# Optimization experiments

Hardware: AMD Instinct MI355X
Metric: run time of the kernel (lower is better)

Reference implementation:

```python
import jax, jax.numpy as jnp
import numpy as np

B, N, D = 16, 1024, 768
H = 12
HD = D // H
HID = 4 * D
EPS = 1e-6


def _layernorm(x, g, b):
    mu = jnp.mean(x, axis=-1, keepdims=True)
    var = jnp.mean(jnp.square(x - mu), axis=-1, keepdims=True)
    return (x - mu) * jax.lax.rsqrt(var + EPS) * g + b


def setup_inputs() -> dict:
    key = jax.random.key(0)
    ks = jax.random.split(key, 8)
    s_d = 1.0 / np.sqrt(D)
    s_h = 1.0 / np.sqrt(HID)
    return {
        "x": jax.random.normal(ks[0], (B, N, D), dtype=jnp.float32),
        "qkv_w": jax.random.uniform(ks[1], (3 * D, D), jnp.float32, -s_d, s_d),
        "proj_w": jax.random.uniform(ks[2], (D, D), jnp.float32, -s_d, s_d),
        "proj_b": jax.random.uniform(ks[3], (D,), jnp.float32, -s_d, s_d),
        "fc1_w": jax.random.uniform(ks[4], (HID, D), jnp.float32, -s_d, s_d),
        "fc1_b": jax.random.uniform(ks[5], (HID,), jnp.float32, -s_d, s_d),
        "fc2_w": jax.random.uniform(ks[6], (D, HID), jnp.float32, -s_h, s_h),
        "fc2_b": jax.random.uniform(ks[7], (D,), jnp.float32, -s_h, s_h),
        "norm1_g": jnp.ones((D,), jnp.float32),
        "norm1_b": jnp.zeros((D,), jnp.float32),
        "norm2_g": jnp.ones((D,), jnp.float32),
        "norm2_b": jnp.zeros((D,), jnp.float32),
    }


def _attention(x, qkv_w, proj_w, proj_b):
    b, n, _ = x.shape
    qkv = x @ qkv_w.T                                  # [b,n,3D] (no bias: qkv_bias=False)
    qkv = qkv.reshape(b, n, 3, H, HD)
    q, k, v = (jnp.transpose(qkv[:, :, i], (0, 2, 1, 3)) for i in range(3))  # [b,h,n,hd]
    scale = HD ** (-0.5)
    dots = jnp.einsum("bhid,bhjd->bhij", q, k) * scale
    attn = jax.nn.softmax(dots, axis=-1)
    out = jnp.einsum("bhij,bhjd->bhid", attn, v)
    out = jnp.transpose(out, (0, 2, 1, 3)).reshape(b, n, H * HD)
    return out @ proj_w.T + proj_b


def _mlp(x, fc1_w, fc1_b, fc2_w, fc2_b):
    h = jax.nn.gelu(x @ fc1_w.T + fc1_b, approximate=False)
    return h @ fc2_w.T + fc2_b


def reference(x, qkv_w, proj_w, proj_b, fc1_w, fc1_b, fc2_w, fc2_b,
              norm1_g, norm1_b, norm2_g, norm2_b):
    x = x + _attention(_layernorm(x, norm1_g, norm1_b), qkv_w, proj_w, proj_b)
    x = x + _mlp(_layernorm(x, norm2_g, norm2_b), fc1_w, fc1_b, fc2_w, fc2_b)
    return x
```

## Files before the change

kernel.cpp:

```cpp
#include <hip/hip_runtime.h>
#include <hip/hip_bf16.h>
#include <math.h>

using bf16 = __hip_bfloat16;
typedef __attribute__((ext_vector_type(8))) short short8;
typedef __attribute__((ext_vector_type(4))) short shortx4;
typedef __attribute__((ext_vector_type(4))) float floatx4;

#define BB 16
#define NN 1024
#define DD 768
#define HH 12
#define HD 64
#define HID 3072

__device__ __forceinline__ floatx4 mfma_bf16(short8 a, short8 b, floatx4 c) {
  return __builtin_amdgcn_mfma_f32_16x16x32_bf16(a, b, c, 0, 0, 0);
}

__device__ __forceinline__ short bf16_bits(float f) {
  union { bf16 h; short s; } u;
  u.h = __float2bfloat16(f);
  return u.s;
}

__device__ __forceinline__ void async_copy16(const void* g, void* l) {
  __builtin_amdgcn_global_load_lds(
      (const __attribute__((address_space(1))) unsigned int*)g,
      (__attribute__((address_space(3))) unsigned int*)l,
      16, 0, 0);
}

__global__ __launch_bounds__(256)
void cvt_kernel(const float* __restrict__ in, bf16* __restrict__ out, int n4)
{
  const int i = blockIdx.x * 256 + threadIdx.x;
  if (i >= n4) return;
  const float4 v = ((const float4*)in)[i];
  shortx4 o;
  o.x = bf16_bits(v.x); o.y = bf16_bits(v.y);
  o.z = bf16_bits(v.z); o.w = bf16_bits(v.w);
  ((shortx4*)out)[i] = o;
}

__global__ __launch_bounds__(256)
void ln_kernel(const float* __restrict__ x, const float* __restrict__ g,
               const float* __restrict__ b, bf16* __restrict__ y)
{
  const int row = blockIdx.x;
  const int t = threadIdx.x;
  const float* xr = x + (size_t)row * DD;
  float v[3];
  float s = 0.f, s2 = 0.f;
#pragma unroll
  for (int i = 0; i < 3; ++i) {
    float f = xr[t + i * 256];
    v[i] = f;
    s += f;
    s2 += f * f;
  }
#pragma unroll
  for (int off = 1; off < 64; off <<= 1) {
    s  += __shfl_xor(s, off);
    s2 += __shfl_xor(s2, off);
  }
  __shared__ float red[2][4];
  const int wave = t >> 6, lane = t & 63;
  if (lane == 0) { red[0][wave] = s; red[1][wave] = s2; }
  __syncthreads();
  s  = red[0][0] + red[0][1] + red[0][2] + red[0][3];
  s2 = red[1][0] + red[1][1] + red[1][2] + red[1][3];
  const float mu = s * (1.f / DD);
  const float var = s2 * (1.f / DD) - mu * mu;
  const float inv = rsqrtf(var + 1e-6f);
  bf16* yr = y + (size_t)row * DD;
#pragma unroll
  for (int i = 0; i < 3; ++i) {
    int c = t + i * 256;
    yr[c] = __float2bfloat16((v[i] - mu) * inv * g[c] + b[c]);
  }
}

template <int EPI>
__global__ __launch_bounds__(256, 4)
void gemm_kernel(const bf16* __restrict__ A, const bf16* __restrict__ W,
                 const float* __restrict__ bias, const float* __restrict__ res,
                 void* __restrict__ Cv, int N, int K)
{
  __shared__ __align__(16) short smem[16896];
  short* sA = smem;
  short* sB = smem + 8192;

  const int tid  = threadIdx.x;
  const int lane = tid & 63;
  const int wave = tid >> 6;
  const int wm = wave & 1, wn = wave >> 1;
  const int row16 = lane & 15, quad = lane >> 4;

  const int lin = blockIdx.y * gridDim.x + blockIdx.x;
  const int per = gridDim.x * 8;
  const int pan = lin / per, rem = lin % per;
  const int bm = (pan * 8 + (rem & 7)) * 128;
  const int bn = (rem >> 3) * 128;

  const int lrow = lane >> 3;
  const int lkc  = (lane & 7) ^ lrow;

  const bf16* Ag = A + (size_t)(bm + wave * 32 + lrow) * K + lkc * 8;
  const bf16* Bg = W + (size_t)(bn + wave * 32 + lrow) * K + lkc * 8;
  short* sAw = sA + wave * 2048;
  short* sBw = sB + wave * 2048;

  floatx4 acc[4][4] = {};

  for (int kt = 0; kt < K; kt += 64) {
#pragma unroll
    for (int g = 0; g < 4; ++g) {
      async_copy16(Ag + (size_t)g * 8 * K + kt, sAw + g * 512);
      async_copy16(Bg + (size_t)g * 8 * K + kt, sBw + g * 512);
    }
    __syncthreads();
#pragma unroll
    for (int c = 0; c < 2; ++c) {
      short8 af[4], bfr[4];
      const int kc = c * 4 + quad;
#pragma unroll
      for (int mt = 0; mt < 4; ++mt) {
        const int row = wm * 64 + mt * 16 + row16;
        af[mt] = *(const short8*)&sA[(row >> 3) * 512 + ((row & 7) * 8 + (kc ^ (row & 7))) * 8];
      }
#pragma unroll
      for (int nt = 0; nt < 4; ++nt) {
        const int row = wn * 64 + nt * 16 + row16;
        bfr[nt] = *(const short8*)&sB[(row >> 3) * 512 + ((row & 7) * 8 + (kc ^ (row & 7))) * 8];
      }
#pragma unroll
      for (int mt = 0; mt < 4; ++mt)
#pragma unroll
        for (int nt = 0; nt < 4; ++nt)
          acc[mt][nt] = mfma_bf16(bfr[nt], af[mt], acc[mt][nt]);
    }
    __syncthreads();
  }

  if (EPI == 1) {
#pragma unroll
    for (int mt = 0; mt < 4; ++mt) {
      const int row = bm + wm * 64 + mt * 16 + row16;
#pragma unroll
      for (int nt = 0; nt < 4; ++nt) {
        const int col = bn + wn * 64 + nt * 16 + quad * 4;
        const floatx4 bv = *(const floatx4*)&bias[col];
        const floatx4 rv = *(const floatx4*)&res[(size_t)row * N + col];
        floatx4 o;
#pragma unroll
        for (int r = 0; r < 4; ++r) o[r] = acc[mt][nt][r] + bv[r] + rv[r];
        *(floatx4*)&((float*)Cv)[(size_t)row * N + col] = o;
      }
    }
  } else {
    short* sC = smem;
#pragma unroll
    for (int mt = 0; mt < 4; ++mt) {
      const int lr = wm * 64 + mt * 16 + row16;
#pragma unroll
      for (int nt = 0; nt < 4; ++nt) {
        const int lc = wn * 64 + nt * 16 + quad * 4;
        floatx4 bv = {};
        if (EPI == 2) bv = *(const floatx4*)&bias[bn + lc];
        shortx4 pk;
#pragma unroll
        for (int r = 0; r < 4; ++r) {
          float v = acc[mt][nt][r] + bv[r];
          if (EPI == 2) v = 0.5f * v * (1.f + erff(v * 0.70710678118f));
          pk[r] = bf16_bits(v);
        }
        *(shortx4*)&sC[lr * 132 + lc] = pk;
      }
    }
    __syncthreads();
#pragma unroll
    for (int it = 0; it < 8; ++it) {
      const int row = (tid >> 4) + it * 16;
      const int col = (tid & 15) * 8;
      short8 v = *(const short8*)&sC[row * 132 + col];
      *(short8*)&((bf16*)Cv)[(size_t)(bm + row) * N + bn + col] = v;
    }
  }
}

__global__ __launch_bounds__(256)
void vtrans_kernel(const bf16* __restrict__ qkv, bf16* __restrict__ vt)
{
  const int bh = blockIdx.y;
  const int b = bh / HH, h = bh % HH;
  const int n0 = blockIdx.x * 64;
  __shared__ __align__(16) short tile[64 * 72];
  const int tid = threadIdx.x;

  const int r = tid >> 2, c16 = (tid & 3) * 16;
  const bf16* src = qkv + (size_t)(b * NN + n0 + r) * 2304 + 2 * DD + h * 64 + c16;
  *(short8*)&tile[r * 72 + c16]     = *(const short8*)(src);
  *(short8*)&tile[r * 72 + c16 + 8] = *(const short8*)(src + 8);
  __syncthreads();

#pragma unroll
  for (int it = 0; it < 2; ++it) {
    const int d  = (tid >> 3) + it * 32;
    const int jg = (tid & 7) * 8;
    short8 o;
#pragma unroll
    for (int t = 0; t < 8; ++t) ((short*)&o)[t] = tile[(jg + t) * 72 + d];
    *(short8*)&vt[((size_t)bh * 64 + d) * NN + n0 + jg] = o;
  }
}

__global__ __launch_bounds__(256, 2)
void attn_kernel(const bf16* __restrict__ qkv, const bf16* __restrict__ vt,
                 bf16* __restrict__ out)
{
  const int bh = blockIdx.y;
  const int b = bh / HH, h = bh % HH;
  const int q0 = blockIdx.x * 128;
  const int tid = threadIdx.x;
  const int lane = tid & 63;
  const int wave = tid >> 6;
  const int row16 = lane & 15, quad = lane >> 4;

  __shared__ __align__(16) short sK[64 * 72];
  __shared__ __align__(16) short sVt[64 * 72];
  __shared__ __align__(16) short sP[4][32 * 72];

  const bf16* base  = qkv + (size_t)b * NN * 2304 + h * 64;
  const bf16* vbase = vt + (size_t)bh * 64 * NN;

  short8 qf[2][2];
#pragma unroll
  for (int qg = 0; qg < 2; ++qg) {
    const bf16* qrow = base + (size_t)(q0 + wave * 32 + qg * 16 + row16) * 2304;
    qf[qg][0] = *(const short8*)(qrow + quad * 8);
    qf[qg][1] = *(const short8*)(qrow + 32 + quad * 8);
  }

  floatx4 o_acc[2][4] = {};
  floatx4 l_acc[2] = {};
  const short8 ones = { (short)0x3F80, (short)0x3F80, (short)0x3F80, (short)0x3F80,
                        (short)0x3F80, (short)0x3F80, (short)0x3F80, (short)0x3F80 };

  const int sr = tid >> 2;
  const int sc = (tid & 3) * 16;
  const float ESC = 0.1803368801f;

  for (int jt = 0; jt < NN / 64; ++jt) {
    const int j0 = jt * 64;
    {
      const bf16* kp = base + (size_t)(j0 + sr) * 2304 + DD + sc;
      *(short8*)&sK[sr * 72 + sc]     = *(const short8*)(kp);
      *(short8*)&sK[sr * 72 + sc + 8] = *(const short8*)(kp + 8);
      const bf16* vp = vbase + (size_t)sr * NN + j0 + sc;
      *(short8*)&sVt[sr * 72 + sc]     = *(const short8*)(vp);
      *(short8*)&sVt[sr * 72 + sc + 8] = *(const short8*)(vp + 8);
    }
    __syncthreads();

#pragma unroll
    for (int nt = 0; nt < 4; ++nt) {
      short8 kb0 = *(const short8*)&sK[(nt * 16 + row16) * 72 + quad * 8];
      short8 kb1 = *(const short8*)&sK[(nt * 16 + row16) * 72 + 32 + quad * 8];
#pragma unroll
      for (int qg = 0; qg < 2; ++qg) {
        floatx4 st = {};
        st = mfma_bf16(kb0, qf[qg][0], st);
        st = mfma_bf16(kb1, qf[qg][1], st);
        shortx4 pk;
#pragma unroll
        for (int r = 0; r < 4; ++r)
          pk[r] = bf16_bits(exp2f(fminf(st[r] * ESC, 30.f)));
        *(shortx4*)&sP[wave][(qg * 16 + row16) * 72 + nt * 16 + quad * 4] = pk;
      }
    }

    short8 vb[4][2];
#pragma unroll
    for (int dt = 0; dt < 4; ++dt) {
      vb[dt][0] = *(const short8*)&sVt[(dt * 16 + row16) * 72 + quad * 8];
      vb[dt][1] = *(const short8*)&sVt[(dt * 16 + row16) * 72 + 32 + quad * 8];
    }
#pragma unroll
    for (int qg = 0; qg < 2; ++qg) {
      short8 pf0 = *(const short8*)&sP[wave][(qg * 16 + row16) * 72 + quad * 8];
      short8 pf1 = *(const short8*)&sP[wave][(qg * 16 + row16) * 72 + 32 + quad * 8];
      l_acc[qg] = mfma_bf16(pf0, ones, l_acc[qg]);
      l_acc[qg] = mfma_bf16(pf1, ones, l_acc[qg]);
#pragma unroll
      for (int dt = 0; dt < 4; ++dt) {
        o_acc[qg][dt] = mfma_bf16(pf0, vb[dt][0], o_acc[qg][dt]);
        o_acc[qg][dt] = mfma_bf16(pf1, vb[dt][1], o_acc[qg][dt]);
      }
    }
    __syncthreads();
  }

#pragma unroll
  for (int qg = 0; qg < 2; ++qg) {
#pragma unroll
    for (int r = 0; r < 4; ++r) {
      const float inv = 1.f / l_acc[qg][r];
      const size_t n = (size_t)(b * NN + q0 + wave * 32 + qg * 16 + quad * 4 + r);
#pragma unroll
      for (int dt = 0; dt < 4; ++dt) {
        out[n * DD + h * 64 + dt * 16 + row16] =
            __float2bfloat16(o_acc[qg][dt][r] * inv);
      }
    }
  }
}

extern "C" void kernel_launch(void* const* d_in, const int* in_sizes, int n_in,
                              void* d_out, int out_size, void* d_ws, size_t ws_size,
                              hipStream_t stream)
{
  const float* x       = (const float*)d_in[0];
  const float* qkv_w   = (const float*)d_in[1];
  const float* proj_w  = (const float*)d_in[2];
  const float* proj_b  = (const float*)d_in[3];
  const float* fc1_w   = (const float*)d_in[4];
  const float* fc1_b   = (const float*)d_in[5];
  const float* fc2_w   = (const float*)d_in[6];
  const float* fc2_b   = (const float*)d_in[7];
  const float* norm1_g = (const float*)d_in[8];
  const float* norm1_b = (const float*)d_in[9];
  const float* norm2_g = (const float*)d_in[10];
  const float* norm2_b = (const float*)d_in[11];
  float* out = (float*)d_out;

  const int M = BB * NN;
  char* ws = (char*)d_ws;

  bf16* wq = (bf16*)ws;
  bf16* wp = wq + (size_t)3 * DD * DD;
  bf16* w1 = wp + (size_t)DD * DD;
  bf16* w2 = w1 + (size_t)HID * DD;
  bf16* xn = w2 + (size_t)DD * HID;
  char* p2 = (char*)(xn + (size_t)M * DD);
  const size_t base_b = (size_t)(p2 - ws);

  int NBc = 1;
  for (int c = 16; c >= 1; c >>= 1)
    if (ws_size >= base_b + (size_t)c * 1024 * 7680) { NBc = c; break; }

  const int Rc = NBc * NN;
  bf16* qkvb = (bf16*)p2;
  bf16* aob  = qkvb + (size_t)Rc * 2304;
  bf16* vtb  = aob  + (size_t)Rc * DD;
  bf16* hb   = (bf16*)p2;

  cvt_kernel<<<(3 * DD * DD / 4 + 255) / 256, 256, 0, stream>>>(qkv_w, wq, 3 * DD * DD / 4);
  cvt_kernel<<<(DD * DD / 4 + 255) / 256, 256, 0, stream>>>(proj_w, wp, DD * DD / 4);
  cvt_kernel<<<(HID * DD / 4 + 255) / 256, 256, 0, stream>>>(fc1_w, w1, HID * DD / 4);
  cvt_kernel<<<(DD * HID / 4 + 255) / 256, 256, 0, stream>>>(fc2_w, w2, DD * HID / 4);

  ln_kernel<<<M, 256, 0, stream>>>(x, norm1_g, norm1_b, xn);

  for (int c = 0; c < BB / NBc; ++c) {
    const size_t r0 = (size_t)c * Rc;
    gemm_kernel<0><<<dim3(3 * DD / 128, Rc / 128), 256, 0, stream>>>(
        xn + r0 * DD, wq, nullptr, nullptr, qkvb, 3 * DD, DD);
    vtrans_kernel<<<dim3(NN / 64, NBc * HH), 256, 0, stream>>>(qkvb, vtb);
    attn_kernel<<<dim3(NN / 128, NBc * HH), 256, 0, stream>>>(qkvb, vtb, aob);
    gemm_kernel<1><<<dim3(DD / 128, Rc / 128), 256, 0, stream>>>(
        aob, wp, proj_b, x + r0 * DD, out + r0 * DD, DD, DD);
  }

  ln_kernel<<<M, 256, 0, stream>>>(out, norm2_g, norm2_b, xn);

  for (int c = 0; c < BB / NBc; ++c) {
    const size_t r0 = (size_t)c * Rc;
    gemm_kernel<2><<<dim3(HID / 128, Rc / 128), 256, 0, stream>>>(
        xn + r0 * DD, w1, fc1_b, nullptr, hb, HID, DD);
    gemm_kernel<1><<<dim3(DD / 128, Rc / 128), 256, 0, stream>>>(
        hb, w2, fc2_b, out + r0 * DD, out + r0 * DD, DD, HID);
  }
}
```

Measured before the change: 556.0 us.

## Rewrite GEMM with 256x256 tiles, 4-stage async LDS pipeline, fast GELU

The GEMM kernel moves from 128x128 tiles with 256 threads and a single-buffered K loop to 256x256 tiles with 512 threads. It uses a 4-slot circular LDS buffer with async global-to-LDS copies, split barriers and s_setprio around the MFMA blocks, so loads for future K-steps overlap compute. The epilogue now writes directly to global memory instead of staging through LDS. The exact erf GELU is replaced by a sigmoid-style exp2/rcp approximation. The changes aim to hide load latency and cut epilogue and transcendental cost, at the price of 128KB LDS per block, fewer blocks in flight, and small numeric differences in GELU.

```diff
diff --git a/kernel.cpp b/kernel.cpp
--- a/kernel.cpp
+++ b/kernel.cpp
@@ -29,6 +29,12 @@
       (const __attribute__((address_space(1))) unsigned int*)g,
       (__attribute__((address_space(3))) unsigned int*)l,
       16, 0, 0);
+}
+
+__device__ __forceinline__ float gelu_f(float x) {
+  const float z = x * fmaf(0.10294324f, x * x, 2.3022082f);
+  const float e = exp2f(z);
+  return x - x * __builtin_amdgcn_rcpf(e + 1.0f);
 }
 
 __global__ __launch_bounds__(256)
@@ -82,109 +88,142 @@
 }
 
 template <int EPI>
-__global__ __launch_bounds__(256, 4)
+__global__ __launch_bounds__(512, 2)
 void gemm_kernel(const bf16* __restrict__ A, const bf16* __restrict__ W,
                  const float* __restrict__ bias, const float* __restrict__ res,
                  void* __restrict__ Cv, int N, int K)
 {
-  __shared__ __align__(16) short smem[16896];
-  short* sA = smem;
-  short* sB = smem + 8192;
+  __shared__ __align__(16) short smem[65536];
 
   const int tid  = threadIdx.x;
   const int lane = tid & 63;
-  const int wave = tid >> 6;
-  const int wm = wave & 1, wn = wave >> 1;
+  const int w    = tid >> 6;
+  const int wm   = w >> 2;
+  const int wn   = w & 3;
   const int row16 = lane & 15, quad = lane >> 4;
 
-  const int lin = blockIdx.y * gridDim.x + blockIdx.x;
-  const int per = gridDim.x * 8;
+  const int gx = gridDim.x, gy = gridDim.y;
+  const int lin = blockIdx.y * gx + blockIdx.x;
+  const int PP  = (gy & 7) ? gy : 8;
+  const int per = gx * PP;
   const int pan = lin / per, rem = lin % per;
-  const int bm = (pan * 8 + (rem & 7)) * 128;
-  const int bn = (rem >> 3) * 128;
-
-  const int lrow = lane >> 3;
-  const int lkc  = (lane & 7) ^ lrow;
-
-  const bf16* Ag = A + (size_t)(bm + wave * 32 + lrow) * K + lkc * 8;
-  const bf16* Bg = W + (size_t)(bn + wave * 32 + lrow) * K + lkc * 8;
-  short* sAw = sA + wave * 2048;
-  short* sBw = sB + wave * 2048;
-
-  floatx4 acc[4][4] = {};
-
-  for (int kt = 0; kt < K; kt += 64) {
-#pragma unroll
-    for (int g = 0; g < 4; ++g) {
-      async_copy16(Ag + (size_t)g * 8 * K + kt, sAw + g * 512);
-      async_copy16(Bg + (size_t)g * 8 * K + kt, sBw + g * 512);
-    }
-    __syncthreads();
-#pragma unroll
-    for (int c = 0; c < 2; ++c) {
-      short8 af[4], bfr[4];
-      const int kc = c * 4 + quad;
-#pragma unroll
-      for (int mt = 0; mt < 4; ++mt) {
-        const int row = wm * 64 + mt * 16 + row16;
-        af[mt] = *(const short8*)&sA[(row >> 3) * 512 + ((row & 7) * 8 + (kc ^ (row & 7))) * 8];
-      }
-#pragma unroll
-      for (int nt = 0; nt < 4; ++nt) {
-        const int row = wn * 64 + nt * 16 + row16;
-        bfr[nt] = *(const short8*)&sB[(row >> 3) * 512 + ((row & 7) * 8 + (kc ^ (row & 7))) * 8];
-      }
-#pragma unroll
-      for (int mt = 0; mt < 4; ++mt)
-#pragma unroll
-        for (int nt = 0; nt < 4; ++nt)
-          acc[mt][nt] = mfma_bf16(bfr[nt], af[mt], acc[mt][nt]);
-    }
-    __syncthreads();
-  }
-
-  if (EPI == 1) {
-#pragma unroll
-    for (int mt = 0; mt < 4; ++mt) {
-      const int row = bm + wm * 64 + mt * 16 + row16;
+  const int bm = (pan * PP + rem % PP) * 256;
+  const int bn = (rem / PP) * 256;
+
+  const int rloc = lane >> 2;
+  const int cl   = lane & 3;
+  const int swzs = (rloc & 3) ^ ((rloc >> 2) & 3);
+  const int cg   = cl ^ swzs;
+  const bf16* Ag = A + (size_t)(bm + w * 32 + rloc) * K + cg * 8;
+  const bf16* Bg = W + (size_t)(bn + w * 32 + rloc) * K + cg * 8;
+  const size_t a16 = (size_t)16 * K;
+  const int stLds = w * 1024;
+
+  const int NS = K >> 5;
+
+  const int swzr = (row16 & 3) ^ ((row16 >> 2) & 3);
+  const int cx   = (quad ^ swzr) * 8;
+
+#define SLOT(u) (((u) & 3) * 16384)
+#define STAGE_A(u, ko) do { \
+    async_copy16(Ag + (ko),        smem + SLOT(u) + stLds); \
+    async_copy16(Ag + a16 + (ko),  smem + SLOT(u) + stLds + 512); } while (0)
+#define STAGE_B(u, ko) do { \
+    async_copy16(Bg + (ko),        smem + SLOT(u) + 8192 + stLds); \
+    async_copy16(Bg + a16 + (ko),  smem + SLOT(u) + 8192 + stLds + 512); } while (0)
+
+  for (int u = 0; u < 3; ++u) {
+    const size_t ko = (size_t)u * 32;
+    STAGE_A(u, ko);
+    STAGE_B(u, ko);
+  }
+
+  floatx4 acc[8][4] = {};
+
+  asm volatile("s_waitcnt vmcnt(8)" ::: "memory");
+  __builtin_amdgcn_s_barrier();
+
+  for (int s = 0; s < NS; ++s) {
+    int u = s + 3; if (u >= NS) u -= NS;
+    const size_t ko = (size_t)u * 32;
+    const short* sAs = smem + SLOT(s);
+    const short* sBs = sAs + 8192;
+
+    short8 af[4], bfr[4];
+#pragma unroll
+    for (int mt = 0; mt < 4; ++mt)
+      af[mt] = *(const short8*)&sAs[(wm * 128 + mt * 16 + row16) * 32 + cx];
+#pragma unroll
+    for (int nt = 0; nt < 4; ++nt)
+      bfr[nt] = *(const short8*)&sBs[(wn * 64 + nt * 16 + row16) * 32 + cx];
+    STAGE_A(u, ko);
+    __builtin_amdgcn_s_barrier();
+    __builtin_amdgcn_s_setprio(1);
+#pragma unroll
+    for (int mt = 0; mt < 4; ++mt)
+#pragma unroll
+      for (int nt = 0; nt < 4; ++nt)
+        acc[mt][nt] = mfma_bf16(bfr[nt], af[mt], acc[mt][nt]);
+    __builtin_amdgcn_s_setprio(0);
+    __builtin_amdgcn_s_barrier();
+
+    short8 af2[4];
+#pragma unroll
+    for (int mt = 0; mt < 4; ++mt)
+      af2[mt] = *(const short8*)&sAs[(wm * 128 + (mt + 4) * 16 + row16) * 32 + cx];
+    STAGE_B(u, ko);
+    __builtin_amdgcn_s_barrier();
+    __builtin_amdgcn_s_setprio(1);
+#pragma unroll
+    for (int mt = 0; mt < 4; ++mt)
+#pragma unroll
+      for (int nt = 0; nt < 4; ++nt)
+        acc[mt + 4][nt] = mfma_bf16(bfr[nt], af2[mt], acc[mt + 4][nt]);
+    __builtin_amdgcn_s_setprio(0);
+    asm volatile("s_waitcnt vmcnt(8)" ::: "memory");
+    __builtin_amdgcn_s_barrier();
+  }
+  asm volatile("s_waitcnt vmcnt(0)" ::: "memory");
+#undef SLOT
+#undef STAGE_A
+#undef STAGE_B
+
+  floatx4 bias4[4] = {};
+  if (EPI != 0) {
+#pragma unroll
+    for (int nt = 0; nt < 4; ++nt)
+      bias4[nt] = *(const floatx4*)&bias[bn + wn * 64 + nt * 16 + quad * 4];
+  }
+
+#pragma unroll
+  for (int mt = 0; mt < 8; ++mt) {
+    const int row = bm + wm * 128 + mt * 16 + row16;
+    if (EPI == 1) {
+      const float* rr = res + (size_t)row * N;
+      float* cr = (float*)Cv + (size_t)row * N;
 #pragma unroll
       for (int nt = 0; nt < 4; ++nt) {
         const int col = bn + wn * 64 + nt * 16 + quad * 4;
-        const floatx4 bv = *(const floatx4*)&bias[col];
-        const floatx4 rv = *(const floatx4*)&res[(size_t)row * N + col];
+        const floatx4 rv = *(const floatx4*)&rr[col];
         floatx4 o;
 #pragma unroll
-        for (int r = 0; r < 4; ++r) o[r] = acc[mt][nt][r] + bv[r] + rv[r];
-        *(floatx4*)&((float*)Cv)[(size_t)row * N + col] = o;
+        for (int r = 0; r < 4; ++r) o[r] = acc[mt][nt][r] + bias4[nt][r] + rv[r];
+        *(floatx4*)&cr[col] = o;
       }
-    }
-  } else {
-    short* sC = smem;
-#pragma unroll
-    for (int mt = 0; mt < 4; ++mt) {
-      const int lr = wm * 64 + mt * 16 + row16;
+    } else {
+      bf16* cr = (bf16*)Cv + (size_t)row * N;
 #pragma unroll
       for (int nt = 0; nt < 4; ++nt) {
-        const int lc = wn * 64 + nt * 16 + quad * 4;
-        floatx4 bv = {};
-        if (EPI == 2) bv = *(const floatx4*)&bias[bn + lc];
+        const int col = bn + wn * 64 + nt * 16 + quad * 4;
         shortx4 pk;
 #pragma unroll
         for (int r = 0; r < 4; ++r) {
-          float v = acc[mt][nt][r] + bv[r];
-          if (EPI == 2) v = 0.5f * v * (1.f + erff(v * 0.70710678118f));
+          float v = acc[mt][nt][r] + bias4[nt][r];
+          if (EPI == 2) v = gelu_f(v);
           pk[r] = bf16_bits(v);
         }
-        *(shortx4*)&sC[lr * 132 + lc] = pk;
+        *(shortx4*)&cr[col] = pk;
       }
-    }
-    __syncthreads();
-#pragma unroll
-    for (int it = 0; it < 8; ++it) {
-      const int row = (tid >> 4) + it * 16;
-      const int col = (tid & 15) * 8;
-      short8 v = *(const short8*)&sC[row * 132 + col];
-      *(short8*)&((bf16*)Cv)[(size_t)(bm + row) * N + bn + col] = v;
     }
   }
 }
@@ -364,11 +403,11 @@
 
   for (int c = 0; c < BB / NBc; ++c) {
     const size_t r0 = (size_t)c * Rc;
-    gemm_kernel<0><<<dim3(3 * DD / 128, Rc / 128), 256, 0, stream>>>(
+    gemm_kernel<0><<<dim3(3 * DD / 256, Rc / 256), 512, 0, stream>>>(
         xn + r0 * DD, wq, nullptr, nullptr, qkvb, 3 * DD, DD);
     vtrans_kernel<<<dim3(NN / 64, NBc * HH), 256, 0, stream>>>(qkvb, vtb);
     attn_kernel<<<dim3(NN / 128, NBc * HH), 256, 0, stream>>>(qkvb, vtb, aob);
-    gemm_kernel<1><<<dim3(DD / 128, Rc / 128), 256, 0, stream>>>(
+    gemm_kernel<1><<<dim3(DD / 256, Rc / 256), 512, 0, stream>>>(
         aob, wp, proj_b, x + r0 * DD, out + r0 * DD, DD, DD);
   }
 
@@ -376,9 +415,9 @@
 
   for (int c = 0; c < BB / NBc; ++c) {
     const size_t r0 = (size_t)c * Rc;
-    gemm_kernel<2><<<dim3(HID / 128, Rc / 128), 256, 0, stream>>>(
+    gemm_kernel<2><<<dim3(HID / 256, Rc / 256), 512, 0, stream>>>(
         xn + r0 * DD, w1, fc1_b, nullptr, hb, HID, DD);
-    gemm_kernel<1><<<dim3(DD / 128, Rc / 128), 256, 0, stream>>>(
+    gemm_kernel<1><<<dim3(DD / 256, Rc / 256), 512, 0, stream>>>(
         hb, w2, fc2_b, out + r0 * DD, out + r0 * DD, DD, HID);
   }
 }
```

Result: slower. 596.7 us (+7.3%).
